# Optimization experiments

Hardware: AMD Instinct MI355X
Metric: run time of the kernel (lower is better)

The kernel has to match this reference:

```python
import jax, jax.numpy as jnp
import numpy as np
import math

NUM_HEADS = 8
FDIM = 64
NUM_BUCKETS = 32
MAX_DISTANCE = 128


def _relative_position_bucket(rel_pos, num_buckets=NUM_BUCKETS, max_distance=MAX_DISTANCE):
    nb = num_buckets // 2
    ret = (rel_pos >= 0).astype(jnp.int32) * nb
    n = jnp.abs(rel_pos)
    max_exact = nb // 2
    is_small = n < max_exact
    # safe log: clamp n to >=1 where large-branch is unused
    val_large = max_exact + (
        jnp.log(jnp.maximum(n, 1).astype(jnp.float32) / max_exact)
        / math.log(max_distance / max_exact) * (nb - max_exact)
    ).astype(jnp.int32)
    val_large = jnp.minimum(val_large, nb - 1)
    return ret + jnp.where(is_small, n, val_large)


def setup_inputs() -> dict:
    key = jax.random.key(0)
    k = jax.random.split(key, 5)
    B, Nin, F, T = 4, 64, FDIM, 1024
    N = NUM_HEADS * FDIM
    x = jax.random.normal(k[0], (B, Nin, F, T), dtype=jnp.float32)
    # kaiming_normal: std = 1/sqrt(fan_in)
    w_in = jax.random.normal(k[1], (NUM_HEADS, Nin), dtype=jnp.float32) / np.sqrt(Nin)
    w_qk = jax.random.normal(k[2], (2 * N, N), dtype=jnp.float32) / np.sqrt(N)
    w_out = jax.random.normal(k[3], (Nin, NUM_HEADS), dtype=jnp.float32) / np.sqrt(NUM_HEADS)
    rel_bias = jax.random.normal(k[4], (NUM_BUCKETS, NUM_HEADS), dtype=jnp.float32) * 0.02
    return {"x": x, "w_in": w_in, "w_qk": w_qk, "w_out": w_out, "rel_bias": rel_bias}


def reference(x, w_in, w_qk, w_out, rel_bias):
    B, Nin, F, T = x.shape
    h, f = NUM_HEADS, FDIM
    scale = f ** (-0.5)
    # proj_in: 1x1 conv2d Nin -> h
    xi = jnp.einsum('bcft,hc->bhft', x, w_in)          # [B,h,F,T]
    xr = xi.reshape(B, h * f, T)                        # b (h f) t
    v = xr.reshape(B, h, f, T).transpose(0, 1, 3, 2)    # [B,h,T,f]
    # qk: 1x1 conv1d N -> 2N
    qk = jnp.einsum('bct,dc->bdt', xr, w_qk)            # [B,2N,T]
    qk = qk.reshape(B, h, 2 * f, T).transpose(0, 1, 3, 2)  # [B,h,T,2f]
    q, k = qk[..., :f], qk[..., f:]
    sim = jnp.einsum('bhnd,bhmd->bhnm', q, k)           # [B,h,T,T]
    # relative position bias
    q_pos = jnp.arange(T)
    k_pos = jnp.arange(T)
    rel = k_pos[None, :] - q_pos[:, None]               # [T,T]
    buckets = _relative_position_bucket(rel)
    bias = rel_bias[buckets]                            # [T,T,h]
    bias = bias.transpose(2, 0, 1)[None]                # [1,h,T,T]
    sim = (sim + bias) * scale
    attn = jax.nn.softmax(sim, axis=-1)
    out = jnp.einsum('bhnm,bhmd->bhnd', attn, v)        # [B,h,T,f]
    out = out.transpose(0, 1, 3, 2)                     # [B,h,f,T]
    out = jnp.einsum('bhft,ch->bcft', out, w_out)       # [B,Nin,F,T]
    return out
```

## Files before the change

### kernel.cpp

```cpp
#include <hip/hip_runtime.h>
#include <math.h>

#define QSCALE 0.18033688011112042f

typedef __attribute__((ext_vector_type(4))) float  f32x4;
typedef __attribute__((ext_vector_type(8))) short  bf16x8;
typedef __attribute__((ext_vector_type(4))) short  bf16x4;
typedef __attribute__((ext_vector_type(4))) int    i32x4;

static __device__ __forceinline__ short f2bf(float f) {
    union { float f; unsigned u; } v; v.f = f;
    unsigned r = v.u + 0x7fffu + ((v.u >> 16) & 1u);
    return (short)(r >> 16);
}

#define MFMA16(A,B,C) __builtin_amdgcn_mfma_f32_16x16x32_bf16(A, B, C, 0, 0, 0)

__global__ void k_prep(const float* __restrict__ wqk, short* __restrict__ wqk_b) {
    int i = blockIdx.x * 256 + threadIdx.x;
    int D = i >> 9;
    float s = (D & 64) ? 1.0f : QSCALE;
    wqk_b[i] = f2bf(wqk[i] * s);
}

__global__ __launch_bounds__(256) void k_proj_in(
    const float* __restrict__ x, const float* __restrict__ w_in,
    short* __restrict__ xi_v, short* __restrict__ xr_t)
{
    __shared__ float w_s[512];
    __shared__ __align__(16) short tr[128 * 72];
    int tid = threadIdx.x;
    int tx = tid & 31, fy = tid >> 5;
    int tb = blockIdx.x, fb = blockIdx.y, b = blockIdx.z;
    w_s[tid] = w_in[tid & 511];
    w_s[tid + 256 & 511] = w_in[tid + 256 & 511];
    __syncthreads();

    int f = fb * 8 + fy;
    int t = tb * 128 + tx * 4;
    float acc[8][4];
    #pragma unroll
    for (int h = 0; h < 8; h++)
        #pragma unroll
        for (int j = 0; j < 4; j++) acc[h][j] = 0.f;

    const float* xp = x + ((size_t)b * 64 * 64 + (size_t)f) * 1024 + t;
    #pragma unroll 8
    for (int c = 0; c < 64; c++) {
        f32x4 xv = *(const f32x4*)&xp[(size_t)c * 65536];
        #pragma unroll
        for (int h = 0; h < 8; h++) {
            float wv = w_s[h * 64 + c];
            #pragma unroll
            for (int j = 0; j < 4; j++) acc[h][j] = fmaf(xv[j], wv, acc[h][j]);
        }
    }
    #pragma unroll
    for (int h = 0; h < 8; h++) {
        bf16x4 pk;
        pk.x = f2bf(acc[h][0]); pk.y = f2bf(acc[h][1]);
        pk.z = f2bf(acc[h][2]); pk.w = f2bf(acc[h][3]);
        *(bf16x4*)&xi_v[(((size_t)b * 8 + h) * 64 + f) * 1024 + t] = pk;
    }
    #pragma unroll
    for (int h = 0; h < 8; h++)
        #pragma unroll
        for (int j = 0; j < 4; j++)
            tr[(tx * 4 + j) * 72 + h * 8 + fy] = f2bf(acc[h][j]);
    __syncthreads();
    int h2 = tid & 7, trow = tid >> 3;
    #pragma unroll
    for (int i = 0; i < 4; i++) {
        int t2 = trow + i * 32;
        i32x4 v = *(const i32x4*)&tr[t2 * 72 + h2 * 8];
        *(i32x4*)&xr_t[((size_t)b * 1024 + tb * 128 + t2) * 512 + h2 * 64 + fb * 8] = v;
    }
}

__global__ __launch_bounds__(256) void k_qk(
    const short* __restrict__ wqk_b, const short* __restrict__ xr_t,
    short* __restrict__ qk_t)
{
    __shared__ __align__(16) short As[128 * 72];
    __shared__ __align__(16) short Bs[64 * 72];
    int tid = threadIdx.x;
    int w = tid >> 6, lane = tid & 63;
    int quad = lane >> 4, l16 = lane & 15;
    int t0 = blockIdx.x * 64;
    int h  = blockIdx.y;
    int b  = blockIdx.z;

    f32x4 acc[2][4];
    #pragma unroll
    for (int r = 0; r < 2; r++)
        #pragma unroll
        for (int tt = 0; tt < 4; tt++) acc[r][tt] = (f32x4){0.f,0.f,0.f,0.f};

    const short* Ag = wqk_b + (size_t)h * 128 * 512;
    const short* Bg = xr_t + ((size_t)b * 1024 + t0) * 512;

    int a_row = tid >> 1, a_col = (tid & 1) * 32;
    int b_row = tid >> 2, b_col = (tid & 3) * 16;

    for (int kk = 0; kk < 512; kk += 64) {
        __syncthreads();
        #pragma unroll
        for (int i = 0; i < 4; i++)
            *(i32x4*)&As[a_row * 72 + a_col + i * 8] =
                *(const i32x4*)&Ag[(size_t)a_row * 512 + kk + a_col + i * 8];
        #pragma unroll
        for (int i = 0; i < 2; i++)
            *(i32x4*)&Bs[b_row * 72 + b_col + i * 8] =
                *(const i32x4*)&Bg[(size_t)b_row * 512 + kk + b_col + i * 8];
        __syncthreads();
        bf16x8 af[2][2];
        #pragma unroll
        for (int r = 0; r < 2; r++)
            #pragma unroll
            for (int kc = 0; kc < 2; kc++)
                af[r][kc] = *(const bf16x8*)&As[(w * 32 + r * 16 + l16) * 72 + kc * 32 + quad * 8];
        #pragma unroll
        for (int tt = 0; tt < 4; tt++) {
            bf16x8 bf0 = *(const bf16x8*)&Bs[(tt * 16 + l16) * 72 + quad * 8];
            bf16x8 bf1 = *(const bf16x8*)&Bs[(tt * 16 + l16) * 72 + 32 + quad * 8];
            #pragma unroll
            for (int r = 0; r < 2; r++) {
                acc[r][tt] = MFMA16(af[r][0], bf0, acc[r][tt]);
                acc[r][tt] = MFMA16(af[r][1], bf1, acc[r][tt]);
            }
        }
    }
    #pragma unroll
    for (int r = 0; r < 2; r++)
        #pragma unroll
        for (int tt = 0; tt < 4; tt++) {
            bf16x4 pk;
            pk.x = f2bf(acc[r][tt][0]); pk.y = f2bf(acc[r][tt][1]);
            pk.z = f2bf(acc[r][tt][2]); pk.w = f2bf(acc[r][tt][3]);
            int t  = t0 + tt * 16 + l16;
            int d2 = w * 32 + r * 16 + quad * 4;
            *(bf16x4*)&qk_t[(((size_t)b * 8 + h) * 1024 + t) * 128 + d2] = pk;
        }
}

__global__ __launch_bounds__(256, 2) void k_attn(
    const short* __restrict__ qk_t, const short* __restrict__ xi_v,
    const float* __restrict__ rel_bias, float* __restrict__ o_t)
{
    __shared__ __align__(16) short Ks[128 * 72];
    __shared__ __align__(16) short Vs[64 * 136];
    __shared__ __align__(16) short Ps[4][16 * 72];
    __shared__ float lut[2048];
    int tid = threadIdx.x;
    int w = tid >> 6, lane = tid & 63;
    int quad = lane >> 4, l16 = lane & 15;
    int nb = blockIdx.x, bh = blockIdx.y;
    int h = bh & 7;
    int n_base = nb * 64;

    for (int i = tid; i < 2047; i += 256) {
        int rel = i - 1023;
        int ret = (rel >= 0) ? 16 : 0;
        int na = rel < 0 ? -rel : rel;
        int idx;
        if (na < 8) idx = ret + na;
        else {
            int vl = 8 + (int)(log2f((float)na * 0.125f) * 2.0f);
            vl = vl > 15 ? 15 : vl;
            idx = ret + vl;
        }
        lut[i] = rel_bias[idx * 8 + h] * QSCALE;
    }

    const short* qb = qk_t + (size_t)bh * (1024 * 128);
    const short* vb = xi_v + (size_t)bh * (64 * 1024);

    bf16x8 qf[2];
    #pragma unroll
    for (int kk = 0; kk < 2; kk++)
        qf[kk] = *(const bf16x8*)&qb[(size_t)(n_base + w * 16 + l16) * 128 + kk * 32 + quad * 8];

    f32x4 acc_o[4];
    #pragma unroll
    for (int dt = 0; dt < 4; dt++) acc_o[dt] = (f32x4){0.f,0.f,0.f,0.f};
    float m_st = -1e30f;
    float l_st = 0.f;

    __syncthreads();

    for (int m0 = 0; m0 < 1024; m0 += 128) {
        {
            int off = (tid & 7) * 8, row = tid >> 3;
            #pragma unroll
            for (int i = 0; i < 4; i++)
                *(i32x4*)&Ks[(row + i * 32) * 72 + off] =
                    *(const i32x4*)&qb[(size_t)(m0 + row + i * 32) * 128 + 64 + off];
            int off2 = (tid & 15) * 8, d = tid >> 4;
            #pragma unroll
            for (int i = 0; i < 4; i++)
                *(i32x4*)&Vs[(d + i * 16) * 136 + off2] =
                    *(const i32x4*)&vb[(size_t)(d + i * 16) * 1024 + m0 + off2];
        }
        __syncthreads();

        f32x4 s[8];
        #pragma unroll
        for (int mt = 0; mt < 8; mt++) {
            bf16x8 kf0 = *(const bf16x8*)&Ks[(mt * 16 + l16) * 72 + quad * 8];
            bf16x8 kf1 = *(const bf16x8*)&Ks[(mt * 16 + l16) * 72 + 32 + quad * 8];
            f32x4 tacc = (f32x4){0.f,0.f,0.f,0.f};
            tacc = MFMA16(kf0, qf[0], tacc);
            tacc = MFMA16(kf1, qf[1], tacc);
            s[mt] = tacc;
        }

        float tmax = -1e30f;
        int n = n_base + w * 16 + l16;
        #pragma unroll
        for (int mt = 0; mt < 8; mt++) {
            int rel0 = m0 + mt * 16 + quad * 4 - n + 1023;
            #pragma unroll
            for (int j = 0; j < 4; j++) {
                float v = s[mt][j] + lut[rel0 + j];
                s[mt][j] = v;
                tmax = fmaxf(tmax, v);
            }
        }
        tmax = fmaxf(tmax, __shfl_xor(tmax, 16));
        tmax = fmaxf(tmax, __shfl_xor(tmax, 32));

        float mnew = fmaxf(m_st, tmax);
        float alpha = exp2f(m_st - mnew);
        m_st = mnew;
        float sum = 0.f;
        #pragma unroll
        for (int mt = 0; mt < 8; mt++)
            #pragma unroll
            for (int j = 0; j < 4; j++) {
                float p = exp2f(s[mt][j] - mnew);
                s[mt][j] = p;
                sum += p;
            }
        sum += __shfl_xor(sum, 16);
        sum += __shfl_xor(sum, 32);
        l_st = l_st * alpha + sum;

        #pragma unroll
        for (int reg = 0; reg < 4; reg++) {
            float a = __shfl(alpha, quad * 4 + reg);
            #pragma unroll
            for (int dt = 0; dt < 4; dt++) acc_o[dt][reg] *= a;
        }
        #pragma unroll
        for (int half = 0; half < 2; half++) {
            #pragma unroll
            for (int mi = 0; mi < 4; mi++) {
                int mt = half * 4 + mi;
                bf16x4 pk;
                pk.x = f2bf(s[mt][0]); pk.y = f2bf(s[mt][1]);
                pk.z = f2bf(s[mt][2]); pk.w = f2bf(s[mt][3]);
                *(bf16x4*)&Ps[w][l16 * 72 + mi * 16 + quad * 4] = pk;
            }
            #pragma unroll
            for (int si = 0; si < 2; si++) {
                bf16x8 pf = *(const bf16x8*)&Ps[w][l16 * 72 + si * 32 + quad * 8];
                #pragma unroll
                for (int dt = 0; dt < 4; dt++) {
                    bf16x8 vf = *(const bf16x8*)&Vs[(dt * 16 + l16) * 136 + half * 64 + si * 32 + quad * 8];
                    acc_o[dt] = MFMA16(pf, vf, acc_o[dt]);
                }
            }
        }
        __syncthreads();
    }
    #pragma unroll
    for (int reg = 0; reg < 4; reg++) {
        float inv = 1.f / __shfl(l_st, quad * 4 + reg);
        #pragma unroll
        for (int dt = 0; dt < 4; dt++) acc_o[dt][reg] *= inv;
    }
    #pragma unroll
    for (int dt = 0; dt < 4; dt++)
        *(f32x4*)&o_t[((size_t)bh * 64 + dt * 16 + l16) * 1024 + n_base + w * 16 + quad * 4] = acc_o[dt];
}

__global__ __launch_bounds__(512) void k_proj_out(
    const float* __restrict__ o_t, const float* __restrict__ w_out,
    float* __restrict__ out)
{
    __shared__ float w_s[512];
    __shared__ float o_s[8][64];
    int tid = threadIdx.x;
    int tx = tid & 63, ty = tid >> 6;
    int tb = blockIdx.x, f = blockIdx.y, b = blockIdx.z;
    w_s[tid] = w_out[tid];
    int t = tb * 64 + tx;
    o_s[ty][tx] = o_t[(((size_t)b * 8 + ty) * 64 + f) * 1024 + t];
    __syncthreads();
    float ov[8];
    #pragma unroll
    for (int hh = 0; hh < 8; hh++) ov[hh] = o_s[hh][tx];
    #pragma unroll
    for (int j = 0; j < 8; j++) {
        int c = ty * 8 + j;
        float a = 0.f;
        #pragma unroll
        for (int hh = 0; hh < 8; hh++) a = fmaf(ov[hh], w_s[c * 8 + hh], a);
        out[(((size_t)b * 64 + c) * 64 + f) * 1024 + t] = a;
    }
}

extern "C" void kernel_launch(void* const* d_in, const int* in_sizes, int n_in,
                              void* d_out, int out_size, void* d_ws, size_t ws_size,
                              hipStream_t stream)
{
    const float* x        = (const float*)d_in[0];
    const float* w_in     = (const float*)d_in[1];
    const float* w_qk     = (const float*)d_in[2];
    const float* w_out    = (const float*)d_in[3];
    const float* rel_bias = (const float*)d_in[4];
    float* out = (float*)d_out;

    char* ws = (char*)d_ws;
    short* wqk_b = (short*)(ws);
    short* xi_v  = (short*)(ws + (size_t)1  * (1 << 20));
    short* xr_t  = (short*)(ws + (size_t)5  * (1 << 20));
    short* qk_t  = (short*)(ws + (size_t)9  * (1 << 20));
    float* o_t   = (float*)(ws + (size_t)17 * (1 << 20));

    hipLaunchKernelGGL(k_prep,     dim3(2048),       dim3(256), 0, stream, w_qk, wqk_b);
    hipLaunchKernelGGL(k_proj_in,  dim3(8, 8, 4),    dim3(256), 0, stream, x, w_in, xi_v, xr_t);
    hipLaunchKernelGGL(k_qk,       dim3(16, 8, 4),   dim3(256), 0, stream, wqk_b, xr_t, qk_t);
    hipLaunchKernelGGL(k_attn,     dim3(16, 32),     dim3(256), 0, stream, qk_t, xi_v, rel_bias, o_t);
    hipLaunchKernelGGL(k_proj_out, dim3(16, 64, 4),  dim3(512), 0, stream, o_t, w_out, out);
}
```

Measured before the change: 193.8 us.

## Split attention along keys, merge partials in proj_out, shrink qk tiles

The attention kernel now splits the key dimension into two halves over a third grid axis. Each half writes an unnormalised partial output plus its running max and sum, and proj_out merges the two halves with log-sum-exp weights before the output projection. The qk GEMM uses 64-row tiles, which doubles its grid, and proj_in software-prefetches the next 8 channel loads into registers. These changes raise the number of blocks and occupancy on a large GPU, at the cost of extra partial-output traffic and merge work.

```diff
diff --git a/kernel.cpp b/kernel.cpp
--- a/kernel.cpp
+++ b/kernel.cpp
@@ -4,6 +4,7 @@
 #define QSCALE 0.18033688011112042f
 
 typedef __attribute__((ext_vector_type(4))) float  f32x4;
+typedef __attribute__((ext_vector_type(2))) float  f32x2;
 typedef __attribute__((ext_vector_type(8))) short  bf16x8;
 typedef __attribute__((ext_vector_type(4))) short  bf16x4;
 typedef __attribute__((ext_vector_type(4))) int    i32x4;
@@ -33,7 +34,7 @@
     int tx = tid & 31, fy = tid >> 5;
     int tb = blockIdx.x, fb = blockIdx.y, b = blockIdx.z;
     w_s[tid] = w_in[tid & 511];
-    w_s[tid + 256 & 511] = w_in[tid + 256 & 511];
+    w_s[(tid + 256) & 511] = w_in[(tid + 256) & 511];
     __syncthreads();
 
     int f = fb * 8 + fy;
@@ -45,15 +46,27 @@
         for (int j = 0; j < 4; j++) acc[h][j] = 0.f;
 
     const float* xp = x + ((size_t)b * 64 * 64 + (size_t)f) * 1024 + t;
-    #pragma unroll 8
-    for (int c = 0; c < 64; c++) {
-        f32x4 xv = *(const f32x4*)&xp[(size_t)c * 65536];
-        #pragma unroll
-        for (int h = 0; h < 8; h++) {
-            float wv = w_s[h * 64 + c];
-            #pragma unroll
-            for (int j = 0; j < 4; j++) acc[h][j] = fmaf(xv[j], wv, acc[h][j]);
-        }
+    f32x4 buf[8];
+    #pragma unroll
+    for (int i = 0; i < 8; i++) buf[i] = *(const f32x4*)&xp[(size_t)i * 65536];
+    #pragma unroll
+    for (int c8 = 0; c8 < 64; c8 += 8) {
+        f32x4 cur[8];
+        #pragma unroll
+        for (int i = 0; i < 8; i++) cur[i] = buf[i];
+        if (c8 + 8 < 64) {
+            #pragma unroll
+            for (int i = 0; i < 8; i++)
+                buf[i] = *(const f32x4*)&xp[(size_t)(c8 + 8 + i) * 65536];
+        }
+        #pragma unroll
+        for (int i = 0; i < 8; i++)
+            #pragma unroll
+            for (int h = 0; h < 8; h++) {
+                float wv = w_s[h * 64 + c8 + i];
+                #pragma unroll
+                for (int j = 0; j < 4; j++) acc[h][j] = fmaf(cur[i][j], wv, acc[h][j]);
+            }
     }
     #pragma unroll
     for (int h = 0; h < 8; h++) {
@@ -77,75 +90,66 @@
     }
 }
 
-__global__ __launch_bounds__(256) void k_qk(
+__global__ __launch_bounds__(256, 4) void k_qk(
     const short* __restrict__ wqk_b, const short* __restrict__ xr_t,
     short* __restrict__ qk_t)
 {
-    __shared__ __align__(16) short As[128 * 72];
+    __shared__ __align__(16) short As[64 * 72];
     __shared__ __align__(16) short Bs[64 * 72];
     int tid = threadIdx.x;
     int w = tid >> 6, lane = tid & 63;
     int quad = lane >> 4, l16 = lane & 15;
     int t0 = blockIdx.x * 64;
-    int h  = blockIdx.y;
+    int Dt = blockIdx.y;
     int b  = blockIdx.z;
 
-    f32x4 acc[2][4];
-    #pragma unroll
-    for (int r = 0; r < 2; r++)
-        #pragma unroll
-        for (int tt = 0; tt < 4; tt++) acc[r][tt] = (f32x4){0.f,0.f,0.f,0.f};
-
-    const short* Ag = wqk_b + (size_t)h * 128 * 512;
+    f32x4 acc[4];
+    #pragma unroll
+    for (int tt = 0; tt < 4; tt++) acc[tt] = (f32x4){0.f,0.f,0.f,0.f};
+
+    const short* Ag = wqk_b + (size_t)Dt * 64 * 512;
     const short* Bg = xr_t + ((size_t)b * 1024 + t0) * 512;
 
-    int a_row = tid >> 1, a_col = (tid & 1) * 32;
-    int b_row = tid >> 2, b_col = (tid & 3) * 16;
+    int s_row = tid >> 2, s_col = (tid & 3) * 16;
 
     for (int kk = 0; kk < 512; kk += 64) {
         __syncthreads();
         #pragma unroll
-        for (int i = 0; i < 4; i++)
-            *(i32x4*)&As[a_row * 72 + a_col + i * 8] =
-                *(const i32x4*)&Ag[(size_t)a_row * 512 + kk + a_col + i * 8];
-        #pragma unroll
-        for (int i = 0; i < 2; i++)
-            *(i32x4*)&Bs[b_row * 72 + b_col + i * 8] =
-                *(const i32x4*)&Bg[(size_t)b_row * 512 + kk + b_col + i * 8];
+        for (int i = 0; i < 2; i++) {
+            *(i32x4*)&As[s_row * 72 + s_col + i * 8] =
+                *(const i32x4*)&Ag[(size_t)s_row * 512 + kk + s_col + i * 8];
+            *(i32x4*)&Bs[s_row * 72 + s_col + i * 8] =
+                *(const i32x4*)&Bg[(size_t)s_row * 512 + kk + s_col + i * 8];
+        }
         __syncthreads();
-        bf16x8 af[2][2];
-        #pragma unroll
-        for (int r = 0; r < 2; r++)
-            #pragma unroll
-            for (int kc = 0; kc < 2; kc++)
-                af[r][kc] = *(const bf16x8*)&As[(w * 32 + r * 16 + l16) * 72 + kc * 32 + quad * 8];
+        bf16x8 af[2];
+        #pragma unroll
+        for (int kc = 0; kc < 2; kc++)
+            af[kc] = *(const bf16x8*)&As[(w * 16 + l16) * 72 + kc * 32 + quad * 8];
         #pragma unroll
         for (int tt = 0; tt < 4; tt++) {
             bf16x8 bf0 = *(const bf16x8*)&Bs[(tt * 16 + l16) * 72 + quad * 8];
             bf16x8 bf1 = *(const bf16x8*)&Bs[(tt * 16 + l16) * 72 + 32 + quad * 8];
-            #pragma unroll
-            for (int r = 0; r < 2; r++) {
-                acc[r][tt] = MFMA16(af[r][0], bf0, acc[r][tt]);
-                acc[r][tt] = MFMA16(af[r][1], bf1, acc[r][tt]);
-            }
-        }
-    }
-    #pragma unroll
-    for (int r = 0; r < 2; r++)
-        #pragma unroll
-        for (int tt = 0; tt < 4; tt++) {
-            bf16x4 pk;
-            pk.x = f2bf(acc[r][tt][0]); pk.y = f2bf(acc[r][tt][1]);
-            pk.z = f2bf(acc[r][tt][2]); pk.w = f2bf(acc[r][tt][3]);
-            int t  = t0 + tt * 16 + l16;
-            int d2 = w * 32 + r * 16 + quad * 4;
-            *(bf16x4*)&qk_t[(((size_t)b * 8 + h) * 1024 + t) * 128 + d2] = pk;
-        }
-}
-
-__global__ __launch_bounds__(256, 2) void k_attn(
+            acc[tt] = MFMA16(af[0], bf0, acc[tt]);
+            acc[tt] = MFMA16(af[1], bf1, acc[tt]);
+        }
+    }
+    int h = Dt >> 1;
+    int d2 = (Dt & 1) * 64 + w * 16 + quad * 4;
+    #pragma unroll
+    for (int tt = 0; tt < 4; tt++) {
+        bf16x4 pk;
+        pk.x = f2bf(acc[tt][0]); pk.y = f2bf(acc[tt][1]);
+        pk.z = f2bf(acc[tt][2]); pk.w = f2bf(acc[tt][3]);
+        int t = t0 + tt * 16 + l16;
+        *(bf16x4*)&qk_t[(((size_t)b * 8 + h) * 1024 + t) * 128 + d2] = pk;
+    }
+}
+
+__global__ __launch_bounds__(256, 3) void k_attn(
     const short* __restrict__ qk_t, const short* __restrict__ xi_v,
-    const float* __restrict__ rel_bias, float* __restrict__ o_t)
+    const float* __restrict__ rel_bias, float* __restrict__ o_part,
+    float* __restrict__ ml)
 {
     __shared__ __align__(16) short Ks[128 * 72];
     __shared__ __align__(16) short Vs[64 * 136];
@@ -154,7 +158,7 @@
     int tid = threadIdx.x;
     int w = tid >> 6, lane = tid & 63;
     int quad = lane >> 4, l16 = lane & 15;
-    int nb = blockIdx.x, bh = blockIdx.y;
+    int nb = blockIdx.x, bh = blockIdx.y, mh = blockIdx.z;
     int h = bh & 7;
     int n_base = nb * 64;
 
@@ -188,7 +192,9 @@
 
     __syncthreads();
 
-    for (int m0 = 0; m0 < 1024; m0 += 128) {
+    #pragma unroll 1
+    for (int it = 0; it < 4; it++) {
+        int m0 = mh * 512 + it * 128;
         {
             int off = (tid & 7) * 8, row = tid >> 3;
             #pragma unroll
@@ -274,19 +280,17 @@
         __syncthreads();
     }
     #pragma unroll
-    for (int reg = 0; reg < 4; reg++) {
-        float inv = 1.f / __shfl(l_st, quad * 4 + reg);
-        #pragma unroll
-        for (int dt = 0; dt < 4; dt++) acc_o[dt][reg] *= inv;
-    }
-    #pragma unroll
     for (int dt = 0; dt < 4; dt++)
-        *(f32x4*)&o_t[((size_t)bh * 64 + dt * 16 + l16) * 1024 + n_base + w * 16 + quad * 4] = acc_o[dt];
+        *(f32x4*)&o_part[(((size_t)mh * 32 + bh) * 64 + dt * 16 + l16) * 1024 + n_base + w * 16 + quad * 4] = acc_o[dt];
+    if (quad == 0) {
+        f32x2 v; v.x = m_st; v.y = l_st;
+        *(f32x2*)&ml[(((size_t)bh * 2 + mh) * 1024 + n_base + w * 16 + l16) * 2] = v;
+    }
 }
 
 __global__ __launch_bounds__(512) void k_proj_out(
-    const float* __restrict__ o_t, const float* __restrict__ w_out,
-    float* __restrict__ out)
+    const float* __restrict__ o_part, const float* __restrict__ ml,
+    const float* __restrict__ w_out, float* __restrict__ out)
 {
     __shared__ float w_s[512];
     __shared__ float o_s[8][64];
@@ -295,7 +299,15 @@
     int tb = blockIdx.x, f = blockIdx.y, b = blockIdx.z;
     w_s[tid] = w_out[tid];
     int t = tb * 64 + tx;
-    o_s[ty][tx] = o_t[(((size_t)b * 8 + ty) * 64 + f) * 1024 + t];
+    int bh = b * 8 + ty;
+    f32x2 ml0 = *(const f32x2*)&ml[(((size_t)bh * 2 + 0) * 1024 + t) * 2];
+    f32x2 ml1 = *(const f32x2*)&ml[(((size_t)bh * 2 + 1) * 1024 + t) * 2];
+    float o0 = o_part[((size_t)(0 * 32 + bh) * 64 + f) * 1024 + t];
+    float o1 = o_part[((size_t)(1 * 32 + bh) * 64 + f) * 1024 + t];
+    float M = fmaxf(ml0.x, ml1.x);
+    float w0 = exp2f(ml0.x - M), w1 = exp2f(ml1.x - M);
+    float inv = 1.f / (ml0.y * w0 + ml1.y * w1);
+    o_s[ty][tx] = (o0 * w0 + o1 * w1) * inv;
     __syncthreads();
     float ov[8];
     #pragma unroll
@@ -322,15 +334,16 @@
     float* out = (float*)d_out;
 
     char* ws = (char*)d_ws;
-    short* wqk_b = (short*)(ws);
-    short* xi_v  = (short*)(ws + (size_t)1  * (1 << 20));
-    short* xr_t  = (short*)(ws + (size_t)5  * (1 << 20));
-    short* qk_t  = (short*)(ws + (size_t)9  * (1 << 20));
-    float* o_t   = (float*)(ws + (size_t)17 * (1 << 20));
+    short* wqk_b  = (short*)(ws);
+    short* xi_v   = (short*)(ws + (size_t)1  * (1 << 20));
+    short* xr_t   = (short*)(ws + (size_t)5  * (1 << 20));
+    short* qk_t   = (short*)(ws + (size_t)9  * (1 << 20));
+    float* o_part = (float*)(ws + (size_t)17 * (1 << 20));
+    float* ml     = (float*)(ws + (size_t)33 * (1 << 20));
 
     hipLaunchKernelGGL(k_prep,     dim3(2048),       dim3(256), 0, stream, w_qk, wqk_b);
     hipLaunchKernelGGL(k_proj_in,  dim3(8, 8, 4),    dim3(256), 0, stream, x, w_in, xi_v, xr_t);
-    hipLaunchKernelGGL(k_qk,       dim3(16, 8, 4),   dim3(256), 0, stream, wqk_b, xr_t, qk_t);
-    hipLaunchKernelGGL(k_attn,     dim3(16, 32),     dim3(256), 0, stream, qk_t, xi_v, rel_bias, o_t);
-    hipLaunchKernelGGL(k_proj_out, dim3(16, 64, 4),  dim3(512), 0, stream, o_t, w_out, out);
-}
+    hipLaunchKernelGGL(k_qk,       dim3(16, 16, 4),  dim3(256), 0, stream, wqk_b, xr_t, qk_t);
+    hipLaunchKernelGGL(k_attn,     dim3(16, 32, 2),  dim3(256), 0, stream, qk_t, xi_v, rel_bias, o_part, ml);
+    hipLaunchKernelGGL(k_proj_out, dim3(16, 64, 4),  dim3(512), 0, stream, o_part, ml, w_out, out);
+}
```

Result: faster. 188.4 us (-2.8%).
